# Kernel tuning notes

Hardware: AMD Instinct MI355X
Metric: run time of the kernel (lower is better)

The kernel has to match this reference:

```python
import jax, jax.numpy as jnp
import numpy as np
import math

SEQ, BATCH, HID, HEADS = 2048, 2, 2048, 16
HEAD_DIM = HID // HEADS
ROPE_BASE = 10000.0


def setup_inputs() -> dict:
    key = jax.random.key(0)
    k1, k2, k3 = jax.random.split(key, 3)
    hidden_states = jax.random.normal(k1, (SEQ, BATCH, HID), dtype=jnp.float32)
    # causal mask: True means masked (gpt2-style attention_mask_func fills with -10000)
    attention_mask = jnp.triu(jnp.ones((SEQ, SEQ), dtype=bool), k=1)[None, None, :, :]
    w_qkv = jax.random.normal(k2, (3 * HID, HID), dtype=jnp.float32) * 0.02
    b_qkv = jnp.zeros((3 * HID,), dtype=jnp.float32)
    w_dense = jax.random.normal(k3, (HID, HID), dtype=jnp.float32) * 0.02
    b_dense = jnp.zeros((HID,), dtype=jnp.float32)
    return {"hidden_states": hidden_states, "attention_mask": attention_mask,
            "w_qkv": w_qkv, "b_qkv": b_qkv, "w_dense": w_dense, "b_dense": b_dense}


def _rotary_cos_sin(seq_len, dim, dtype):
    inv_freq = 1.0 / (ROPE_BASE ** (jnp.arange(0, dim, 2, dtype=jnp.float32) / dim))
    t = jnp.arange(seq_len, dtype=jnp.float32)
    freqs = jnp.einsum("s,d->sd", t, inv_freq)
    emb = jnp.concatenate([freqs, freqs], axis=-1)  # [s, dim]
    # broadcast to [s, 1, 1, dim] over (batch, heads)
    return jnp.cos(emb)[:, None, None, :].astype(dtype), jnp.sin(emb)[:, None, None, :].astype(dtype)


def _rotate_half(x):
    x1, x2 = jnp.split(x, 2, axis=-1)
    return jnp.concatenate([-x2, x1], axis=-1)


def reference(hidden_states, attention_mask, w_qkv, b_qkv, w_dense, b_dense):
    s, b, h = hidden_states.shape
    # QKV projection: [s, b, 3h] -> [s, b, nh, 3*hd] -> split
    mixed = hidden_states @ w_qkv.T + b_qkv
    mixed = mixed.reshape(s, b, HEADS, 3 * HEAD_DIM)
    q, k, v = jnp.split(mixed, 3, axis=-1)  # each [s, b, nh, hd]
    # rotary (rotary_pct == 1 -> full head dim)
    cos, sin = _rotary_cos_sin(s, HEAD_DIM, q.dtype)
    q = q * cos + _rotate_half(q) * sin
    k = k * cos + _rotate_half(k) * sin
    # attention scores [b, nh, s_q, s_k]
    norm_factor = math.sqrt(HEAD_DIM)
    scores = jnp.einsum("sbhd,tbhd->bhst", q, k) / norm_factor
    scores = jnp.where(attention_mask, jnp.asarray(-10000.0, scores.dtype), scores)
    # softmax in fp32
    probs = jax.nn.softmax(scores.astype(jnp.float32), axis=-1).astype(scores.dtype)
    # context [s, b, nh, hd] -> [s, b, h]
    context = jnp.einsum("bhst,tbhd->sbhd", probs, v).reshape(s, b, h)
    # dense with skip_bias_add: bias returned separately
    output = context @ w_dense.T
    return output, b_dense
```

## Files before the change

### kernel.cpp

```cpp
#include <hip/hip_runtime.h>
#include <cstdint>
#include <math.h>


typedef unsigned short u16;
typedef __bf16 bf16x8 __attribute__((ext_vector_type(8)));
typedef float floatx4 __attribute__((ext_vector_type(4)));

#define SEQ 2048
#define BATCH 2
#define HID 2048
#define NH 16
#define HD 128

__device__ __forceinline__ u16 f2bf(float f) {
  union { float f; uint32_t u; } v; v.f = f;
  uint32_t u = v.u;
  return (u16)((u + 0x7FFFu + ((u >> 16) & 1u)) >> 16);
}

__device__ __forceinline__ void st8_bf16(u16* dst, const float* s) {
  uint32_t pk[4];
#pragma unroll
  for (int j = 0; j < 4; j++)
    pk[j] = (uint32_t)f2bf(s[2 * j]) | ((uint32_t)f2bf(s[2 * j + 1]) << 16);
  *(uint4*)dst = make_uint4(pk[0], pk[1], pk[2], pk[3]);
}

__device__ __forceinline__ void gl16(const u16* g, u16* l) {
  __builtin_amdgcn_global_load_lds(
      (const __attribute__((address_space(1))) void*)g,
      (__attribute__((address_space(3))) void*)l, 16, 0, 0);
}

__global__ __launch_bounds__(256) void cvt_inputs(
    const float* __restrict__ W, const float* __restrict__ Hid,
    u16* __restrict__ wb, u16* __restrict__ Ah, u16* __restrict__ wvw) {
  const int blk = blockIdx.x;
  const int c0 = threadIdx.x * 8;
  const float* src;
  u16* dst;
  if (blk < 4096) {
    int dt = blk >> 7, r = blk & 127;
    int srow = (dt < 16) ? ((dt * 3 + 1) * 128 + r) : (((dt - 16) * 3) * 128 + r);
    src = W + (size_t)srow * HID;
    dst = wb + (size_t)blk * HID;
  } else if (blk < 8192) {
    int r = blk - 4096;
    src = Hid + (size_t)r * HID;
    dst = Ah + (size_t)r * HID;
  } else {
    int v = blk - 8192;
    int h = v >> 7, r = v & 127;
    src = W + (size_t)((h * 3 + 2) * 128 + r) * HID;
    dst = wvw + (size_t)v * HID;
  }
  float t[8];
  *(floatx4*)&t[0] = *(const floatx4*)(src + c0);
  *(floatx4*)&t[4] = *(const floatx4*)(src + c0 + 4);
  st8_bf16(dst + c0, t);
}

__global__ __launch_bounds__(256) void cvt_wd(const float* __restrict__ W,
                                              u16* __restrict__ wd) {
  const int r = blockIdx.x;
  const int c0 = threadIdx.x * 8;
  float t[8];
  const float* src = W + (size_t)r * HID;
  *(floatx4*)&t[0] = *(const floatx4*)(src + c0);
  *(floatx4*)&t[4] = *(const floatx4*)(src + c0 + 4);
  st8_bf16(wd + (size_t)r * HID + c0, t);
}

__global__ __launch_bounds__(256, 2) void qkv_qk(
    const u16* __restrict__ Ah, const u16* __restrict__ wb,
    const float* __restrict__ bias, u16* __restrict__ Qw,
    u16* __restrict__ Kw) {
  __shared__ __align__(16) u16 As[128 * 64];
  __shared__ __align__(16) u16 Bs[128 * 64];
  const int tid = threadIdx.x;
  const int wv = tid >> 6, lane = tid & 63;
  const int quad = lane >> 4, l16 = lane & 15;
  const int wt = blockIdx.x;
  const int bm = blockIdx.y;
  const int rowA0 = bm * 128;
  const int wm = (wv >> 1) * 64;
  const int wn = (wv & 1) * 32;
  const int ntoff[4] = {wn, wn + 16, wn + 64, wn + 80};

  const int lrow = wv * 32 + (lane >> 3);
  const int lcol = (lane & 7) * 8;
  const u16* Ag = Ah + (size_t)(rowA0 + lrow) * HID + lcol;
  const u16* Bg = wb + ((size_t)wt * 128 + lrow) * HID + lcol;
  u16* Al = &As[(wv * 32) * 64];
  u16* Bl = &Bs[(wv * 32) * 64];

  floatx4 acc[4][4];
#pragma unroll
  for (int i = 0; i < 4; i++)
#pragma unroll
    for (int j = 0; j < 4; j++) acc[i][j] = (floatx4){0.f, 0.f, 0.f, 0.f};

  for (int kb = 0; kb < HID; kb += 64) {
#pragma unroll
    for (int j = 0; j < 4; j++) {
      gl16(Ag + (size_t)j * 8 * HID + kb, Al + j * 8 * 64);
      gl16(Bg + (size_t)j * 8 * HID + kb, Bl + j * 8 * 64);
    }
    __syncthreads();
#pragma unroll
    for (int ks = 0; ks < 64; ks += 32) {
      bf16x8 af[4], bfr[4];
#pragma unroll
      for (int mi = 0; mi < 4; mi++)
        af[mi] = *(const bf16x8*)&As[(wm + mi * 16 + l16) * 64 + ks + quad * 8];
#pragma unroll
      for (int ni = 0; ni < 4; ni++)
        bfr[ni] = *(const bf16x8*)&Bs[(ntoff[ni] + l16) * 64 + ks + quad * 8];
#pragma unroll
      for (int mi = 0; mi < 4; mi++)
#pragma unroll
        for (int ni = 0; ni < 4; ni++)
          acc[mi][ni] = __builtin_amdgcn_mfma_f32_16x16x32_bf16(
              af[mi], bfr[ni], acc[mi][ni], 0, 0, 0);
    }
    __syncthreads();
  }

  const int seg = (wt < 16) ? 1 : 0;
  const int head = wt & 15;
  u16* dst = seg ? Kw : Qw;
  float bv[4];
#pragma unroll
  for (int ni = 0; ni < 4; ni++)
    bv[ni] = bias[(head * 3 + seg) * 128 + ntoff[ni] + l16];
  const float RC = 0.20762050593045951f;
  const float f0 = exp2f(-(float)(wn + l16) * RC);
  const float f1 = exp2f(-(float)(wn + 16 + l16) * RC);

#pragma unroll
  for (int mi = 0; mi < 4; mi++) {
#pragma unroll
    for (int reg = 0; reg < 4; reg++) {
      int r = rowA0 + wm + mi * 16 + quad * 4 + reg;
      int s = r >> 1, b = r & 1;
      size_t base = ((size_t)(b * NH + head) * SEQ + s) * HD;
      float sv, cv;
      sincosf((float)s * f0, &sv, &cv);
      {
        float lo = acc[mi][0][reg] + bv[0];
        float hi = acc[mi][2][reg] + bv[2];
        dst[base + wn + l16] = f2bf(lo * cv - hi * sv);
        dst[base + wn + l16 + 64] = f2bf(hi * cv + lo * sv);
      }
      sincosf((float)s * f1, &sv, &cv);
      {
        float lo = acc[mi][1][reg] + bv[1];
        float hi = acc[mi][3][reg] + bv[3];
        dst[base + wn + 16 + l16] = f2bf(lo * cv - hi * sv);
        dst[base + wn + 16 + l16 + 64] = f2bf(hi * cv + lo * sv);
      }
    }
  }
}

__global__ __launch_bounds__(256, 2) void qkv_v(
    const u16* __restrict__ Ah, const u16* __restrict__ wvw,
    const float* __restrict__ bias, u16* __restrict__ Vt) {
  __shared__ __align__(16) u16 As[128 * 64];
  __shared__ __align__(16) u16 Bs[128 * 64];
  const int tid = threadIdx.x;
  const int wv = tid >> 6, lane = tid & 63;
  const int quad = lane >> 4, l16 = lane & 15;
  const int head = blockIdx.x;
  const int bm = blockIdx.y;
  const int rowA0 = bm * 128;
  const int wm = (wv >> 1) * 64;
  const int wn = (wv & 1) * 32;
  const int ntoff[4] = {wn, wn + 16, wn + 64, wn + 80};

  const int lrow = wv * 32 + (lane >> 3);
  const int lcol = (lane & 7) * 8;
  const u16* Ag = Ah + (size_t)(rowA0 + lrow) * HID + lcol;
  const u16* Bg = wvw + ((size_t)head * 128 + lrow) * HID + lcol;
  u16* Al = &As[(wv * 32) * 64];
  u16* Bl = &Bs[(wv * 32) * 64];

  floatx4 acc[4][4];
#pragma unroll
  for (int i = 0; i < 4; i++)
#pragma unroll
    for (int j = 0; j < 4; j++) acc[i][j] = (floatx4){0.f, 0.f, 0.f, 0.f};

  for (int kb = 0; kb < HID; kb += 64) {
#pragma unroll
    for (int j = 0; j < 4; j++) {
      gl16(Ag + (size_t)j * 8 * HID + kb, Al + j * 8 * 64);
      gl16(Bg + (size_t)j * 8 * HID + kb, Bl + j * 8 * 64);
    }
    __syncthreads();
#pragma unroll
    for (int ks = 0; ks < 64; ks += 32) {
      bf16x8 af[4], bfr[4];
#pragma unroll
      for (int mi = 0; mi < 4; mi++)
        af[mi] = *(const bf16x8*)&As[(wm + mi * 16 + l16) * 64 + ks + quad * 8];
#pragma unroll
      for (int ni = 0; ni < 4; ni++)
        bfr[ni] = *(const bf16x8*)&Bs[(ntoff[ni] + l16) * 64 + ks + quad * 8];
#pragma unroll
      for (int mi = 0; mi < 4; mi++)
#pragma unroll
        for (int ni = 0; ni < 4; ni++)
          acc[mi][ni] = __builtin_amdgcn_mfma_f32_16x16x32_bf16(
              af[mi], bfr[ni], acc[mi][ni], 0, 0, 0);
    }
    __syncthreads();
  }

  float bv[4];
#pragma unroll
  for (int ni = 0; ni < 4; ni++)
    bv[ni] = bias[(head * 3 + 2) * 128 + ntoff[ni] + l16];
#pragma unroll
  for (int mi = 0; mi < 4; mi++) {
#pragma unroll
    for (int ni = 0; ni < 4; ni++) {
      int d = ntoff[ni] + l16;
#pragma unroll
      for (int reg = 0; reg < 4; reg++) {
        int r = rowA0 + wm + mi * 16 + quad * 4 + reg;
        int s = r >> 1, b = r & 1;
        Vt[((size_t)(b * NH + head) * HD + d) * SEQ + s] =
            f2bf(acc[mi][ni][reg] + bv[ni]);
      }
    }
  }
}

__global__ __launch_bounds__(256, 2) void attn(
    const u16* __restrict__ Qw, const u16* __restrict__ Kw,
    const u16* __restrict__ Vt, u16* __restrict__ ctx) {
  __shared__ __align__(16) u16 Ks[2][64 * 128];
  __shared__ __align__(16) u16 Vs[2][128 * 64];
  __shared__ __align__(16) u16 Pl[4][32 * 64];

  const int tid = threadIdx.x;
  const int wv = tid >> 6, lane = tid & 63;
  const int quad = lane >> 4, l16 = lane & 15;
  const int bh = blockIdx.y;
  const int b = bh >> 4, h = bh & 15;
  const int qt = (bh < 16) ? blockIdx.x : 15 - blockIdx.x;
  const int sw = qt * 128 + wv * 32;
  const size_t bhoff = (size_t)bh * SEQ * HD;

  bf16x8 qf[2][4];
#pragma unroll
  for (int mi = 0; mi < 2; mi++)
#pragma unroll
    for (int kc = 0; kc < 4; kc++)
      qf[mi][kc] = *(const bf16x8*)&Qw[bhoff +
                                       (size_t)(sw + mi * 16 + l16) * HD +
                                       kc * 32 + quad * 8];

  floatx4 o[2][8];
#pragma unroll
  for (int mi = 0; mi < 2; mi++)
#pragma unroll
    for (int ni = 0; ni < 8; ni++) o[mi][ni] = (floatx4){0.f, 0.f, 0.f, 0.f};
  float mst[2][4], lst[2][4];
#pragma unroll
  for (int mi = 0; mi < 2; mi++)
#pragma unroll
    for (int r = 0; r < 4; r++) { mst[mi][r] = -1e30f; lst[mi][r] = 0.f; }

  const int nt = qt * 2 + 2;
  const float SCL2 = 0.088388347648318447f * 1.442695040888963f;
  const float MSK2 = -10000.0f * 1.442695040888963f;
  const float THR = 8.0f;

#define STAGE(bb, tt)                                                          \
  {                                                                            \
    _Pragma("unroll") for (int i = 0; i < 4; i++) {                            \
      int c = i * 256 + tid;                                                   \
      int rk = c >> 4, uk = c & 15;                                            \
      gl16(&Kw[bhoff + (size_t)((tt) * 64 + rk) * HD + (uk ^ (rk & 7)) * 8],   \
           &Ks[bb][(i * 256 + wv * 64) * 8]);                                  \
      int rv_ = c >> 3, uv = c & 7;                                            \
      gl16(&Vt[bhoff + (size_t)rv_ * SEQ + (tt) * 64 + (uv ^ (rv_ & 7)) * 8],  \
           &Vs[bb][(i * 256 + wv * 64) * 8]);                                  \
    }                                                                          \
  }

  STAGE(0, 0);
  __syncthreads();

  for (int t = 0; t < nt; t++) {
    const int cur = t & 1;
    if (t + 1 < nt) STAGE(cur ^ 1, t + 1);

    const bool active = (t * 64 <= sw + 31);
    if (active) {
      const bool diag = (t * 64 + 63 > sw);
      floatx4 sa[2][4];
#pragma unroll
      for (int mi = 0; mi < 2; mi++)
#pragma unroll
        for (int ni = 0; ni < 4; ni++) sa[mi][ni] = (floatx4){0.f, 0.f, 0.f, 0.f};
      __builtin_amdgcn_s_setprio(1);
#pragma unroll
      for (int kc = 0; kc < 4; kc++) {
        bf16x8 kf[4];
#pragma unroll
        for (int ni = 0; ni < 4; ni++)
          kf[ni] = *(const bf16x8*)&Ks[cur][(ni * 16 + l16) * 128 +
                                            (((kc * 4 + quad) ^ (l16 & 7)) * 8)];
#pragma unroll
        for (int mi = 0; mi < 2; mi++)
#pragma unroll
          for (int ni = 0; ni < 4; ni++)
            sa[mi][ni] = __builtin_amdgcn_mfma_f32_16x16x32_bf16(
                qf[mi][kc], kf[ni], sa[mi][ni], 0, 0, 0);
      }
      __builtin_amdgcn_s_setprio(0);

      float alpha[2][4];
      int anyr = 0;
#pragma unroll
      for (int mi = 0; mi < 2; mi++) {
#pragma unroll
        for (int reg = 0; reg < 4; reg++) {
          const int rr = mi * 16 + quad * 4 + reg;
          const int sq = sw + rr;
          float rv[4];
          if (diag) {
#pragma unroll
            for (int ni = 0; ni < 4; ni++) {
              int sk = t * 64 + ni * 16 + l16;
              float v = sa[mi][ni][reg] * SCL2;
              if (sk > sq) v = MSK2;
              rv[ni] = v;
            }
          } else {
#pragma unroll
            for (int ni = 0; ni < 4; ni++) rv[ni] = sa[mi][ni][reg] * SCL2;
          }
          float rmax = fmaxf(fmaxf(rv[0], rv[1]), fmaxf(rv[2], rv[3]));
          rmax = fmaxf(rmax, __shfl_xor(rmax, 1));
          rmax = fmaxf(rmax, __shfl_xor(rmax, 2));
          rmax = fmaxf(rmax, __shfl_xor(rmax, 4));
          rmax = fmaxf(rmax, __shfl_xor(rmax, 8));
          float al;
          if (__all(rmax <= mst[mi][reg] + THR)) {
            al = 1.0f;
          } else {
            float mn = fmaxf(mst[mi][reg], rmax);
            al = exp2f(mst[mi][reg] - mn);
            mst[mi][reg] = mn;
            anyr = 1;
          }
          const float m0 = mst[mi][reg];
          float rs = 0.f;
#pragma unroll
          for (int ni = 0; ni < 4; ni++) {
            float p = exp2f(rv[ni] - m0);
            rs += p;
            Pl[wv][rr * 64 + ((ni * 16 + l16) ^ ((rr & 7) << 3))] = f2bf(p);
          }
          rs += __shfl_xor(rs, 1);
          rs += __shfl_xor(rs, 2);
          rs += __shfl_xor(rs, 4);
          rs += __shfl_xor(rs, 8);
          lst[mi][reg] = lst[mi][reg] * al + rs;
          alpha[mi][reg] = al;
        }
      }
      if (anyr) {
#pragma unroll
        for (int mi = 0; mi < 2; mi++)
#pragma unroll
          for (int ni = 0; ni < 8; ni++)
#pragma unroll
            for (int reg = 0; reg < 4; reg++)
              o[mi][ni][reg] *= alpha[mi][reg];
      }

      __builtin_amdgcn_s_setprio(1);
#pragma unroll
      for (int kc = 0; kc < 2; kc++) {
        bf16x8 pf[2];
#pragma unroll
        for (int mi = 0; mi < 2; mi++)
          pf[mi] = *(const bf16x8*)&Pl[wv][(mi * 16 + l16) * 64 +
                                           ((kc * 32 + quad * 8) ^
                                            ((l16 & 7) << 3))];
#pragma unroll
        for (int ni = 0; ni < 8; ni++) {
          bf16x8 vf = *(const bf16x8*)&Vs[cur][(ni * 16 + l16) * 64 +
                                               (((kc * 4 + quad) ^ (l16 & 7)) *
                                                8)];
#pragma unroll
          for (int mi = 0; mi < 2; mi++)
            o[mi][ni] = __builtin_amdgcn_mfma_f32_16x16x32_bf16(
                pf[mi], vf, o[mi][ni], 0, 0, 0);
        }
      }
      __builtin_amdgcn_s_setprio(0);
    }
    __syncthreads();
  }

#pragma unroll
  for (int mi = 0; mi < 2; mi++) {
#pragma unroll
    for (int reg = 0; reg < 4; reg++) {
      float inv = 1.0f / lst[mi][reg];
      int sq = sw + mi * 16 + quad * 4 + reg;
      size_t rbase = ((size_t)(sq * BATCH + b)) * HID + h * HD;
#pragma unroll
      for (int ni = 0; ni < 8; ni++)
        ctx[rbase + ni * 16 + l16] = f2bf(o[mi][ni][reg] * inv);
    }
  }
#undef STAGE
}

__global__ __launch_bounds__(256, 2) void dense_gemm(
    const u16* __restrict__ A, const u16* __restrict__ Wd,
    float* __restrict__ out) {
  __shared__ __align__(16) u16 As[128 * 64];
  __shared__ __align__(16) u16 Bs[128 * 64];
  const int tid = threadIdx.x;
  const int wv = tid >> 6, lane = tid & 63;
  const int quad = lane >> 4, l16 = lane & 15;
  const int bn = blockIdx.x, bm = blockIdx.y;
  const int rowA0 = bm * 128, rowB0 = bn * 128;
  const int wm = (wv >> 1) * 64;
  const int wn = (wv & 1) * 64;
  const int ntoff[4] = {wn, wn + 16, wn + 32, wn + 48};

  const int lrow = wv * 32 + (lane >> 3);
  const int lcol = (lane & 7) * 8;
  const u16* Ag = A + (size_t)(rowA0 + lrow) * HID + lcol;
  const u16* Bg = Wd + (size_t)(rowB0 + lrow) * HID + lcol;
  u16* Al = &As[(wv * 32) * 64];
  u16* Bl = &Bs[(wv * 32) * 64];

  floatx4 acc[4][4];
#pragma unroll
  for (int i = 0; i < 4; i++)
#pragma unroll
    for (int j = 0; j < 4; j++) acc[i][j] = (floatx4){0.f, 0.f, 0.f, 0.f};

  for (int kb = 0; kb < HID; kb += 64) {
#pragma unroll
    for (int j = 0; j < 4; j++) {
      gl16(Ag + (size_t)j * 8 * HID + kb, Al + j * 8 * 64);
      gl16(Bg + (size_t)j * 8 * HID + kb, Bl + j * 8 * 64);
    }
    __syncthreads();
#pragma unroll
    for (int ks = 0; ks < 64; ks += 32) {
      bf16x8 af[4], bfr[4];
#pragma unroll
      for (int mi = 0; mi < 4; mi++)
        af[mi] = *(const bf16x8*)&As[(wm + mi * 16 + l16) * 64 + ks + quad * 8];
#pragma unroll
      for (int ni = 0; ni < 4; ni++)
        bfr[ni] = *(const bf16x8*)&Bs[(ntoff[ni] + l16) * 64 + ks + quad * 8];
#pragma unroll
      for (int mi = 0; mi < 4; mi++)
#pragma unroll
        for (int ni = 0; ni < 4; ni++)
          acc[mi][ni] = __builtin_amdgcn_mfma_f32_16x16x32_bf16(
              af[mi], bfr[ni], acc[mi][ni], 0, 0, 0);
    }
    __syncthreads();
  }

#pragma unroll
  for (int mi = 0; mi < 4; mi++)
#pragma unroll
    for (int reg = 0; reg < 4; reg++) {
      int r = rowA0 + wm + mi * 16 + quad * 4 + reg;
#pragma unroll
      for (int ni = 0; ni < 4; ni++)
        out[(size_t)r * HID + bn * 128 + ntoff[ni] + l16] = acc[mi][ni][reg];
    }
}

__global__ void copy_bias(const float* __restrict__ bd, float* __restrict__ out) {
  int i = blockIdx.x * 256 + threadIdx.x;
  if (i < HID) out[(size_t)SEQ * BATCH * HID + i] = bd[i];
}

extern "C" void kernel_launch(void* const* d_in, const int* in_sizes, int n_in,
                              void* d_out, int out_size, void* d_ws,
                              size_t ws_size, hipStream_t stream) {
  const float *hidden = nullptr, *w_qkv = nullptr, *b_qkv = nullptr;
  const float *w_dense = nullptr, *b_dense = nullptr;
  for (int i = 0; i < n_in; i++) {
    long s = in_sizes[i];
    if (s == 8388608L) hidden = (const float*)d_in[i];
    else if (s == 12582912L) w_qkv = (const float*)d_in[i];
    else if (s == 6144L) b_qkv = (const float*)d_in[i];
    else if (s == 4194304L) w_dense = (const float*)d_in[i];
    else if (s == 2048L) b_dense = (const float*)d_in[i];
  }
  float* out = (float*)d_out;

  char* ws = (char*)d_ws;
  u16* Qw = (u16*)(ws);
  u16* Kw = (u16*)(ws + 16777216ll);
  u16* Vt = (u16*)(ws + 33554432ll);
  u16* wb = (u16*)(ws + 33554432ll);
  u16* Ah = (u16*)(ws + 50331648ll);
  u16* ctx = (u16*)(ws + 50331648ll);
  u16* wd = (u16*)(ws);
  u16* wvw = (u16*)d_out;

  cvt_inputs<<<dim3(10240), dim3(256), 0, stream>>>(w_qkv, hidden, wb, Ah, wvw);
  qkv_qk<<<dim3(32, 32), dim3(256), 0, stream>>>(Ah, wb, b_qkv, Qw, Kw);
  qkv_v<<<dim3(16, 32), dim3(256), 0, stream>>>(Ah, wvw, b_qkv, Vt);
  attn<<<dim3(16, 32), dim3(256), 0, stream>>>(Qw, Kw, Vt, ctx);
  cvt_wd<<<dim3(2048), dim3(256), 0, stream>>>(w_dense, wd);
  dense_gemm<<<dim3(16, 32), dim3(256), 0, stream>>>(ctx, wd, out);
  copy_bias<<<dim3(8), dim3(256), 0, stream>>>(b_dense, out);
}
```

Measured before the change: 474.5 us.

## Split long causal query tiles across KV halves and merge with combine kernel

Query tiles 9-15 are now split into two work items, each covering half of the key range. They write unnormalized partial outputs plus running max and sum to scratch space in the output buffer, and a new combine kernel merges them. The grid grows from 16 to 23 items per batch-head and is ordered longest-first, to even out the causal load imbalance across workgroups. In exchange, the K/V shared-memory double buffering is dropped in favour of a single buffer with two barriers per tile, which exposes load latency, and there is extra fp32 partial traffic plus one more launch.

Measured after the change: 486.9 us. 1.03x slower.

```diff
diff --git a/kernel.cpp b/kernel.cpp
--- a/kernel.cpp
+++ b/kernel.cpp
@@ -238,11 +238,17 @@
   }
 }
 
+__constant__ int qtA[23] = {8, 15, 15, 7, 14, 14, 13, 13, 6, 12, 12, 11,
+                            11, 5, 10, 10, 9, 9, 4, 3, 2, 1, 0};
+__constant__ int khA[23] = {2, 0, 1, 2, 0, 1, 0, 1, 2, 0, 1, 0,
+                            1, 2, 0, 1, 0, 1, 2, 2, 2, 2, 2};
+
 __global__ __launch_bounds__(256, 2) void attn(
     const u16* __restrict__ Qw, const u16* __restrict__ Kw,
-    const u16* __restrict__ Vt, u16* __restrict__ ctx) {
-  __shared__ __align__(16) u16 Ks[2][64 * 128];
-  __shared__ __align__(16) u16 Vs[2][128 * 64];
+    const u16* __restrict__ Vt, u16* __restrict__ ctx,
+    float* __restrict__ po, float* __restrict__ pml) {
+  __shared__ __align__(16) u16 Ks[64 * 128];
+  __shared__ __align__(16) u16 Vs[128 * 64];
   __shared__ __align__(16) u16 Pl[4][32 * 64];
 
   const int tid = threadIdx.x;
@@ -250,7 +256,11 @@
   const int quad = lane >> 4, l16 = lane & 15;
   const int bh = blockIdx.y;
   const int b = bh >> 4, h = bh & 15;
-  const int qt = (bh < 16) ? blockIdx.x : 15 - blockIdx.x;
+  const int item = blockIdx.x;
+  const int qt = qtA[item];
+  const int kh = khA[item];
+  const int t0 = (kh == 2) ? 0 : kh * (qt + 1);
+  const int t1 = (kh == 2) ? (2 * qt + 2) : (t0 + qt + 1);
   const int sw = qt * 128 + wv * 32;
   const size_t bhoff = (size_t)bh * SEQ * HD;
 
@@ -274,30 +284,27 @@
 #pragma unroll
     for (int r = 0; r < 4; r++) { mst[mi][r] = -1e30f; lst[mi][r] = 0.f; }
 
-  const int nt = qt * 2 + 2;
   const float SCL2 = 0.088388347648318447f * 1.442695040888963f;
   const float MSK2 = -10000.0f * 1.442695040888963f;
   const float THR = 8.0f;
 
-#define STAGE(bb, tt)                                                          \
+#define STAGE(tt)                                                              \
   {                                                                            \
     _Pragma("unroll") for (int i = 0; i < 4; i++) {                            \
       int c = i * 256 + tid;                                                   \
       int rk = c >> 4, uk = c & 15;                                            \
       gl16(&Kw[bhoff + (size_t)((tt) * 64 + rk) * HD + (uk ^ (rk & 7)) * 8],   \
-           &Ks[bb][(i * 256 + wv * 64) * 8]);                                  \
+           &Ks[(i * 256 + wv * 64) * 8]);                                      \
       int rv_ = c >> 3, uv = c & 7;                                            \
       gl16(&Vt[bhoff + (size_t)rv_ * SEQ + (tt) * 64 + (uv ^ (rv_ & 7)) * 8],  \
-           &Vs[bb][(i * 256 + wv * 64) * 8]);                                  \
+           &Vs[(i * 256 + wv * 64) * 8]);                                      \
     }                                                                          \
   }
 
-  STAGE(0, 0);
-  __syncthreads();
-
-  for (int t = 0; t < nt; t++) {
-    const int cur = t & 1;
-    if (t + 1 < nt) STAGE(cur ^ 1, t + 1);
+  for (int t = t0; t < t1; t++) {
+    __syncthreads();
+    STAGE(t);
+    __syncthreads();
 
     const bool active = (t * 64 <= sw + 31);
     if (active) {
@@ -313,8 +320,8 @@
         bf16x8 kf[4];
 #pragma unroll
         for (int ni = 0; ni < 4; ni++)
-          kf[ni] = *(const bf16x8*)&Ks[cur][(ni * 16 + l16) * 128 +
-                                            (((kc * 4 + quad) ^ (l16 & 7)) * 8)];
+          kf[ni] = *(const bf16x8*)&Ks[(ni * 16 + l16) * 128 +
+                                       (((kc * 4 + quad) ^ (l16 & 7)) * 8)];
 #pragma unroll
         for (int mi = 0; mi < 2; mi++)
 #pragma unroll
@@ -396,9 +403,8 @@
                                             ((l16 & 7) << 3))];
 #pragma unroll
         for (int ni = 0; ni < 8; ni++) {
-          bf16x8 vf = *(const bf16x8*)&Vs[cur][(ni * 16 + l16) * 64 +
-                                               (((kc * 4 + quad) ^ (l16 & 7)) *
-                                                8)];
+          bf16x8 vf = *(const bf16x8*)&Vs[(ni * 16 + l16) * 64 +
+                                          (((kc * 4 + quad) ^ (l16 & 7)) * 8)];
 #pragma unroll
           for (int mi = 0; mi < 2; mi++)
             o[mi][ni] = __builtin_amdgcn_mfma_f32_16x16x32_bf16(
@@ -407,22 +413,72 @@
       }
       __builtin_amdgcn_s_setprio(0);
     }
-    __syncthreads();
-  }
-
-#pragma unroll
-  for (int mi = 0; mi < 2; mi++) {
-#pragma unroll
-    for (int reg = 0; reg < 4; reg++) {
-      float inv = 1.0f / lst[mi][reg];
-      int sq = sw + mi * 16 + quad * 4 + reg;
-      size_t rbase = ((size_t)(sq * BATCH + b)) * HID + h * HD;
-#pragma unroll
-      for (int ni = 0; ni < 8; ni++)
-        ctx[rbase + ni * 16 + l16] = f2bf(o[mi][ni][reg] * inv);
+  }
+
+  if (kh == 2) {
+#pragma unroll
+    for (int mi = 0; mi < 2; mi++) {
+#pragma unroll
+      for (int reg = 0; reg < 4; reg++) {
+        float inv = 1.0f / lst[mi][reg];
+        int sq = sw + mi * 16 + quad * 4 + reg;
+        size_t rbase = ((size_t)(sq * BATCH + b)) * HID + h * HD;
+#pragma unroll
+        for (int ni = 0; ni < 8; ni++)
+          ctx[rbase + ni * 16 + l16] = f2bf(o[mi][ni][reg] * inv);
+      }
+    }
+  } else {
+    const int pidx = (bh * 7 + (qt - 9)) * 2 + kh;
+    float* ob = po + (size_t)pidx * 16384;
+#pragma unroll
+    for (int mi = 0; mi < 2; mi++) {
+#pragma unroll
+      for (int reg = 0; reg < 4; reg++) {
+        int row = wv * 32 + mi * 16 + quad * 4 + reg;
+#pragma unroll
+        for (int ni = 0; ni < 8; ni++)
+          ob[row * 128 + ni * 16 + l16] = o[mi][ni][reg];
+        if (l16 == 0) {
+          pml[pidx * 256 + row * 2] = mst[mi][reg];
+          pml[pidx * 256 + row * 2 + 1] = lst[mi][reg];
+        }
+      }
     }
   }
 #undef STAGE
+}
+
+__global__ __launch_bounds__(256) void combine(const float* __restrict__ po,
+                                               const float* __restrict__ pml,
+                                               u16* __restrict__ ctx) {
+  const int bh = blockIdx.y;
+  const int qi = blockIdx.x;
+  const int qt = 9 + qi;
+  const int b = bh >> 4, h = bh & 15;
+  const int p0 = (bh * 7 + qi) * 2;
+  const int tid = threadIdx.x;
+  const int row = tid >> 1;
+  const int d0 = (tid & 1) * 64;
+  const float m1 = pml[p0 * 256 + row * 2];
+  const float l1 = pml[p0 * 256 + row * 2 + 1];
+  const float m2 = pml[(p0 + 1) * 256 + row * 2];
+  const float l2 = pml[(p0 + 1) * 256 + row * 2 + 1];
+  const float mm = fmaxf(m1, m2);
+  const float w1 = exp2f(m1 - mm), w2 = exp2f(m2 - mm);
+  const float inv = 1.0f / (l1 * w1 + l2 * w2);
+  const float* o1 = po + (size_t)p0 * 16384 + row * 128 + d0;
+  const float* o2 = po + (size_t)(p0 + 1) * 16384 + row * 128 + d0;
+  const int sq = qt * 128 + row;
+  u16* cb = ctx + ((size_t)(sq * BATCH + b)) * HID + h * HD + d0;
+#pragma unroll
+  for (int j = 0; j < 16; j++) {
+    floatx4 a = *(const floatx4*)(o1 + j * 4);
+    floatx4 c = *(const floatx4*)(o2 + j * 4);
+#pragma unroll
+    for (int e = 0; e < 4; e++)
+      cb[j * 4 + e] = f2bf((a[e] * w1 + c[e] * w2) * inv);
+  }
 }
 
 __global__ __launch_bounds__(256, 2) void dense_gemm(
@@ -518,11 +574,14 @@
   u16* ctx = (u16*)(ws + 50331648ll);
   u16* wd = (u16*)(ws);
   u16* wvw = (u16*)d_out;
+  float* po = (float*)d_out;
+  float* pml = (float*)d_out + 7340032;
 
   cvt_inputs<<<dim3(10240), dim3(256), 0, stream>>>(w_qkv, hidden, wb, Ah, wvw);
   qkv_qk<<<dim3(32, 32), dim3(256), 0, stream>>>(Ah, wb, b_qkv, Qw, Kw);
   qkv_v<<<dim3(16, 32), dim3(256), 0, stream>>>(Ah, wvw, b_qkv, Vt);
-  attn<<<dim3(16, 32), dim3(256), 0, stream>>>(Qw, Kw, Vt, ctx);
+  attn<<<dim3(23, 32), dim3(256), 0, stream>>>(Qw, Kw, Vt, ctx, po, pml);
+  combine<<<dim3(7, 32), dim3(256), 0, stream>>>(po, pml, ctx);
   cvt_wd<<<dim3(2048), dim3(256), 0, stream>>>(w_dense, wd);
   dense_gemm<<<dim3(16, 32), dim3(256), 0, stream>>>(ctx, wd, out);
   copy_bias<<<dim3(8), dim3(256), 0, stream>>>(b_dense, out);
```

## Single-buffer attention K/V tiles and remap blocks across XCDs

Applied to the files above, without the earlier changes.

The attention kernel drops its double-buffered K/V shared memory and now stages one tile per iteration, with a barrier before and after each load. LDS per block falls from about 80KB to about 48KB, which could let more blocks fit per CU. Block indices are also remapped so consecutive linear block IDs spread across the 8 XCDs by batch-head, with the causal tile order alternating to balance work. The cost is that global loads no longer overlap compute, so each iteration stalls on its own load.

Result: no change. 469.5 us (-1.1%).

```diff
diff --git a/kernel.cpp b/kernel.cpp
--- a/kernel.cpp
+++ b/kernel.cpp
@@ -241,16 +241,23 @@
 __global__ __launch_bounds__(256, 2) void attn(
     const u16* __restrict__ Qw, const u16* __restrict__ Kw,
     const u16* __restrict__ Vt, u16* __restrict__ ctx) {
-  __shared__ __align__(16) u16 Ks[2][64 * 128];
-  __shared__ __align__(16) u16 Vs[2][128 * 64];
+  __shared__ __align__(16) u16 Ks[64 * 128];
+  __shared__ __align__(16) u16 Vs[128 * 64];
   __shared__ __align__(16) u16 Pl[4][32 * 64];
 
   const int tid = threadIdx.x;
   const int wv = tid >> 6, lane = tid & 63;
   const int quad = lane >> 4, l16 = lane & 15;
-  const int bh = blockIdx.y;
+
+  const int lin = blockIdx.y * gridDim.x + blockIdx.x;
+  const int xcdsel = lin & 7;
+  const int k = lin >> 3;
+  const int bh_hi = k >> 4;
+  const int x = k & 15;
+  const int bh = (bh_hi << 3) | xcdsel;
+  const int qt = ((bh_hi >> 1) & 1) ? (15 - x) : x;
+
   const int b = bh >> 4, h = bh & 15;
-  const int qt = (bh < 16) ? blockIdx.x : 15 - blockIdx.x;
   const int sw = qt * 128 + wv * 32;
   const size_t bhoff = (size_t)bh * SEQ * HD;
 
@@ -279,25 +286,23 @@
   const float MSK2 = -10000.0f * 1.442695040888963f;
   const float THR = 8.0f;
 
-#define STAGE(bb, tt)                                                          \
+#define STAGE(tt)                                                              \
   {                                                                            \
     _Pragma("unroll") for (int i = 0; i < 4; i++) {                            \
       int c = i * 256 + tid;                                                   \
       int rk = c >> 4, uk = c & 15;                                            \
       gl16(&Kw[bhoff + (size_t)((tt) * 64 + rk) * HD + (uk ^ (rk & 7)) * 8],   \
-           &Ks[bb][(i * 256 + wv * 64) * 8]);                                  \
+           &Ks[(i * 256 + wv * 64) * 8]);                                      \
       int rv_ = c >> 3, uv = c & 7;                                            \
       gl16(&Vt[bhoff + (size_t)rv_ * SEQ + (tt) * 64 + (uv ^ (rv_ & 7)) * 8],  \
-           &Vs[bb][(i * 256 + wv * 64) * 8]);                                  \
+           &Vs[(i * 256 + wv * 64) * 8]);                                      \
     }                                                                          \
   }
 
-  STAGE(0, 0);
-  __syncthreads();
-
   for (int t = 0; t < nt; t++) {
-    const int cur = t & 1;
-    if (t + 1 < nt) STAGE(cur ^ 1, t + 1);
+    __syncthreads();
+    STAGE(t);
+    __syncthreads();
 
     const bool active = (t * 64 <= sw + 31);
     if (active) {
@@ -313,8 +318,8 @@
         bf16x8 kf[4];
 #pragma unroll
         for (int ni = 0; ni < 4; ni++)
-          kf[ni] = *(const bf16x8*)&Ks[cur][(ni * 16 + l16) * 128 +
-                                            (((kc * 4 + quad) ^ (l16 & 7)) * 8)];
+          kf[ni] = *(const bf16x8*)&Ks[(ni * 16 + l16) * 128 +
+                                       (((kc * 4 + quad) ^ (l16 & 7)) * 8)];
 #pragma unroll
         for (int mi = 0; mi < 2; mi++)
 #pragma unroll
@@ -396,9 +401,8 @@
                                             ((l16 & 7) << 3))];
 #pragma unroll
         for (int ni = 0; ni < 8; ni++) {
-          bf16x8 vf = *(const bf16x8*)&Vs[cur][(ni * 16 + l16) * 64 +
-                                               (((kc * 4 + quad) ^ (l16 & 7)) *
-                                                8)];
+          bf16x8 vf = *(const bf16x8*)&Vs[(ni * 16 + l16) * 64 +
+                                          (((kc * 4 + quad) ^ (l16 & 7)) * 8)];
 #pragma unroll
           for (int mi = 0; mi < 2; mi++)
             o[mi][ni] = __builtin_amdgcn_mfma_f32_16x16x32_bf16(
@@ -407,7 +411,6 @@
       }
       __builtin_amdgcn_s_setprio(0);
     }
-    __syncthreads();
   }
 
 #pragma unroll
```
